# Kernel tuning notes

Measured on AMD Instinct MI355X. Metric: run time of the kernel, lower is better.

The kernel has to match this reference:

```python
import jax, jax.numpy as jnp
import numpy as np

N_NODES = 50000
N_EDGES = 800000
D_IN = 128
D_HID = 128
D_OUT = 128
EPS = 0.1  # GINConv eps


def setup_inputs() -> dict:
    key = jax.random.key(0)
    k = jax.random.split(key, 8)
    scale = 1.0 / np.sqrt(D_IN)
    return {
        "x": jax.random.normal(k[0], (N_NODES, D_IN), dtype=jnp.float32),
        "edge_index": jax.random.randint(k[1], (2, N_EDGES), 0, N_NODES, dtype=jnp.int64),
        "edge_weight": jax.random.uniform(k[2], (N_EDGES,), dtype=jnp.float32),
        "W1a": jax.random.normal(k[3], (D_IN, D_HID), dtype=jnp.float32) * scale,
        "W1b": jax.random.normal(k[4], (D_HID, D_HID), dtype=jnpp.float32) if False else jax.random.normal(k[4], (D_HID, D_HID), dtype=jnp.float32) * scale,
        "W2a": jax.random.normal(k[5], (D_HID, D_HID), dtype=jnp.float32) * scale,
        "W2b": jax.random.normal(k[6], (D_HID, D_OUT), dtype=jnp.float32) * scale,
    }


def _gin_conv(h, src, dst, ew, Wa, Wb, n_nodes):
    # edge-weighted neighbor sum: aggr[i] = sum_{(j->i)} w_ji * h[j]
    msg = ew[:, None] * h[src]                       # [E, d]
    aggr = jax.ops.segment_sum(msg, dst, num_segments=n_nodes)  # [N, d]
    z = (1.0 + EPS) * h + aggr                       # GIN update
    # 2-layer bias-free MLP: lin -> relu -> lin
    return jnp.maximum(z @ Wa, 0.0) @ Wb


def reference(x, edge_index, edge_weight, W1a, W1b, W2a, W2b):
    src, dst = edge_index[0], edge_index[1]
    n = x.shape[0]
    h = _gin_conv(x, src, dst, edge_weight, W1a, W1b, n)
    h = jnp.maximum(h, 0.0)  # relu between convs; dropout is identity in eval
    h = _gin_conv(h, src, dst, edge_weight, W2a, W2b, n)
    return h
```

## Files before the change

### kernel.cpp

```cpp
#include <hip/hip_runtime.h>
#include <hip/hip_fp16.h>

#define D 128
#define N_NODES 50000
#define EPSP1 1.1f

#define NPB 128
#define NBUCK 391
#define CAP 2560
#define P1E 4096
#define TS 136

typedef __attribute__((ext_vector_type(8))) short short8;
typedef __attribute__((ext_vector_type(4))) float f32x4;

__device__ __forceinline__ unsigned short f2bf(float f) {
    unsigned u = __float_as_uint(f);
    u += 0x7FFF + ((u >> 16) & 1);
    return (unsigned short)(u >> 16);
}
__device__ __forceinline__ float bf2f(unsigned short h) {
    return __uint_as_float(((unsigned)h) << 16);
}

__global__ __launch_bounds__(512, 4) void pass1_all(
    const int* __restrict__ src, const int* __restrict__ dst,
    const float* __restrict__ ew, int* __restrict__ gcnt,
    uint2* __restrict__ gstage, int ne, int nb1,
    const float* __restrict__ x, unsigned short* __restrict__ hb,
    int n4, int ncvt,
    const float* __restrict__ W1a, const float* __restrict__ W1b,
    const float* __restrict__ W2a, const float* __restrict__ W2b,
    unsigned short* __restrict__ wp)
{
    __shared__ int bcnt[NBUCK];
    __shared__ int goff[NBUCK];
    int tid = threadIdx.x;
    int bid = blockIdx.x;

    if (bid < nb1) {
        for (int i = tid; i < NBUCK; i += 512) bcnt[i] = 0;
        __syncthreads();
        int e0 = bid * P1E;
        int   rank[8];
        int   buck[8];
        uint2 pay[8];
#pragma unroll
        for (int j = 0; j < 8; ++j) {
            int e = e0 + j * 512 + tid;
            buck[j] = -1;
            if (e < ne) {
                int d_ = dst[e];
                int b  = d_ >> 7;
                int dl = d_ & 127;
                pay[j].x = (unsigned)(src[e] & 0xFFFF) | ((unsigned)dl << 16);
                pay[j].y = (unsigned)__half_as_ushort(__float2half_rn(ew[e]));
                rank[j]  = atomicAdd(&bcnt[b], 1);
                buck[j]  = b;
            }
        }
        __syncthreads();
        for (int i = tid; i < NBUCK; i += 512)
            if (bcnt[i] > 0) goff[i] = atomicAdd(&gcnt[i], bcnt[i]);
        __syncthreads();
#pragma unroll
        for (int j = 0; j < 8; ++j) {
            if (buck[j] >= 0) {
                int pos = goff[buck[j]] + rank[j];
                if (pos < CAP)
                    gstage[(size_t)buck[j] * CAP + pos] = pay[j];
            }
        }
    } else if (bid < nb1 + ncvt) {
        int base = (bid - nb1) * 4096;
#pragma unroll
        for (int it = 0; it < 8; ++it) {
            int i = base + it * 512 + tid;
            if (i < n4) {
                float4 v = ((const float4*)x)[i];
                ushort4 o;
                o.x = f2bf(v.x); o.y = f2bf(v.y); o.z = f2bf(v.z); o.w = f2bf(v.w);
                ((ushort4*)hb)[i] = o;
            }
        }
    } else {
        int e2 = (bid - nb1 - ncvt) * 512 + tid;
        if (e2 < 8192) {
            int mat = e2 >> 11;
            int e   = e2 & 2047;
            const float* W = (mat == 0) ? W1a : (mat == 1) ? W1b : (mat == 2) ? W2a : W2b;
            unsigned short* Wp = wp + (size_t)mat * 16384;
            int col = e & 127;
            int kq  = e >> 7;
            short8 v;
#pragma unroll
            for (int j = 0; j < 8; ++j)
                v[j] = (short)f2bf(W[(size_t)(kq * 8 + j) * 128 + col]);
            ((short8*)Wp)[e] = v;
        }
    }
}

__global__ __launch_bounds__(512) void csr_build(
    const uint2* __restrict__ gstage, const int* __restrict__ gcnt,
    unsigned* __restrict__ epay, int* __restrict__ off)
{
    __shared__ int hist[NPB];
    __shared__ int scn[NPB];
    __shared__ int exc[NPB];
    __shared__ int wtot[2];
    __shared__ int base_s;

    int b = blockIdx.x;
    int t = threadIdx.x;
    int cnt = min(gcnt[b], CAP);

    if (t < NPB) hist[t] = 0;
    __syncthreads();

    uint2 ent[CAP / 512];
    int   rnk[CAP / 512];
#pragma unroll
    for (int it = 0; it < CAP / 512; ++it) {
        int i = it * 512 + t;
        if (i < cnt) {
            ent[it] = gstage[(size_t)b * CAP + i];
            rnk[it] = atomicAdd(&hist[(ent[it].x >> 16) & 255], 1);
        }
    }
    __syncthreads();

    int w = t >> 6, l = t & 63;
    if (w < 2) {
        int v = hist[w * 64 + l];
#pragma unroll
        for (int dd = 1; dd < 64; dd <<= 1) {
            int u = __shfl_up(v, dd, 64);
            if (l >= dd) v += u;
        }
        scn[w * 64 + l] = v;
        if (l == 63) wtot[w] = v;
    } else if (w == 2) {
        int v = 0;
        for (int i = l; i < NBUCK; i += 64)
            if (i < b) v += min(gcnt[i], CAP);
#pragma unroll
        for (int dd = 32; dd > 0; dd >>= 1) v += __shfl_down(v, dd, 64);
        if (l == 0) base_s = v;
    }
    __syncthreads();

    if (t < NPB) {
        int pre = (t >= 64) ? wtot[0] : 0;
        int incl = scn[t] + pre;
        int excl = incl - hist[t];
        int node = (b << 7) + t;
        if (node <= N_NODES) off[node] = base_s + excl;
        exc[t] = excl;
    }
    __syncthreads();

    int base_s_r = base_s;
#pragma unroll
    for (int it = 0; it < CAP / 512; ++it) {
        int i = it * 512 + t;
        if (i < cnt) {
            int dl = (ent[it].x >> 16) & 255;
            epay[base_s_r + exc[dl] + rnk[it]] =
                (ent[it].x & 0xFFFF) | (ent[it].y << 16);
        }
    }
}

template<int RELU2, int OUT_F32>
__global__ __launch_bounds__(512, 8) void conv_fused(
    const unsigned short* __restrict__ h, const int* __restrict__ off,
    const unsigned* __restrict__ epay,
    const unsigned short* __restrict__ WpA,
    const unsigned short* __restrict__ WpB,
    void* __restrict__ outv, int n)
{
    __shared__ unsigned short t1[32 * TS];
    __shared__ unsigned short t2[32 * TS];
    __shared__ int offs[33];

    int tid  = threadIdx.x;
    int wave = tid >> 6;
    int lane = tid & 63;
    int qtr  = lane >> 4;
    int sub  = lane & 15;
    int nb   = blockIdx.x * 32;

    if (tid < 33) offs[tid] = off[min(nb + tid, n)];
    __syncthreads();

    int row  = wave * 4 + qtr;
    int node = nb + row;
    int beg = offs[row];
    int end = offs[row + 1];

    float acc[8];
#pragma unroll
    for (int c = 0; c < 8; ++c) acc[c] = 0.f;

    int i = beg;
    for (; i + 8 <= end; i += 8) {
        unsigned p0 = epay[i];
        unsigned p1 = epay[i + 1];
        unsigned p2 = epay[i + 2];
        unsigned p3 = epay[i + 3];
        unsigned p4 = epay[i + 4];
        unsigned p5 = epay[i + 5];
        unsigned p6 = epay[i + 6];
        unsigned p7 = epay[i + 7];
        short8 v0 = ((const short8*)(h + (size_t)(p0 & 0xFFFF) * D))[sub];
        short8 v1 = ((const short8*)(h + (size_t)(p1 & 0xFFFF) * D))[sub];
        short8 v2 = ((const short8*)(h + (size_t)(p2 & 0xFFFF) * D))[sub];
        short8 v3 = ((const short8*)(h + (size_t)(p3 & 0xFFFF) * D))[sub];
        short8 v4 = ((const short8*)(h + (size_t)(p4 & 0xFFFF) * D))[sub];
        short8 v5 = ((const short8*)(h + (size_t)(p5 & 0xFFFF) * D))[sub];
        short8 v6 = ((const short8*)(h + (size_t)(p6 & 0xFFFF) * D))[sub];
        short8 v7 = ((const short8*)(h + (size_t)(p7 & 0xFFFF) * D))[sub];
        float w0 = __half2float(__ushort_as_half((unsigned short)(p0 >> 16)));
        float w1 = __half2float(__ushort_as_half((unsigned short)(p1 >> 16)));
        float w2 = __half2float(__ushort_as_half((unsigned short)(p2 >> 16)));
        float w3 = __half2float(__ushort_as_half((unsigned short)(p3 >> 16)));
        float w4 = __half2float(__ushort_as_half((unsigned short)(p4 >> 16)));
        float w5 = __half2float(__ushort_as_half((unsigned short)(p5 >> 16)));
        float w6 = __half2float(__ushort_as_half((unsigned short)(p6 >> 16)));
        float w7 = __half2float(__ushort_as_half((unsigned short)(p7 >> 16)));
#pragma unroll
        for (int c = 0; c < 8; ++c)
            acc[c] += w0 * bf2f((unsigned short)v0[c]) + w1 * bf2f((unsigned short)v1[c])
                    + w2 * bf2f((unsigned short)v2[c]) + w3 * bf2f((unsigned short)v3[c])
                    + w4 * bf2f((unsigned short)v4[c]) + w5 * bf2f((unsigned short)v5[c])
                    + w6 * bf2f((unsigned short)v6[c]) + w7 * bf2f((unsigned short)v7[c]);
    }
    for (; i + 4 <= end; i += 4) {
        unsigned p0 = epay[i];
        unsigned p1 = epay[i + 1];
        unsigned p2 = epay[i + 2];
        unsigned p3 = epay[i + 3];
        short8 v0 = ((const short8*)(h + (size_t)(p0 & 0xFFFF) * D))[sub];
        short8 v1 = ((const short8*)(h + (size_t)(p1 & 0xFFFF) * D))[sub];
        short8 v2 = ((const short8*)(h + (size_t)(p2 & 0xFFFF) * D))[sub];
        short8 v3 = ((const short8*)(h + (size_t)(p3 & 0xFFFF) * D))[sub];
        float w0 = __half2float(__ushort_as_half((unsigned short)(p0 >> 16)));
        float w1 = __half2float(__ushort_as_half((unsigned short)(p1 >> 16)));
        float w2 = __half2float(__ushort_as_half((unsigned short)(p2 >> 16)));
        float w3 = __half2float(__ushort_as_half((unsigned short)(p3 >> 16)));
#pragma unroll
        for (int c = 0; c < 8; ++c)
            acc[c] += w0 * bf2f((unsigned short)v0[c]) + w1 * bf2f((unsigned short)v1[c])
                    + w2 * bf2f((unsigned short)v2[c]) + w3 * bf2f((unsigned short)v3[c]);
    }
    for (; i < end; ++i) {
        unsigned p0 = epay[i];
        short8 v0 = ((const short8*)(h + (size_t)(p0 & 0xFFFF) * D))[sub];
        float w0 = __half2float(__ushort_as_half((unsigned short)(p0 >> 16)));
#pragma unroll
        for (int c = 0; c < 8; ++c)
            acc[c] += w0 * bf2f((unsigned short)v0[c]);
    }

    {
        const short8 zero8 = {0, 0, 0, 0, 0, 0, 0, 0};
        short8 o;
        if (node < n) {
            short8 xv = ((const short8*)(h + (size_t)node * D))[sub];
#pragma unroll
            for (int c = 0; c < 8; ++c)
                o[c] = (short)f2bf(acc[c] + EPSP1 * bf2f((unsigned short)xv[c]));
        } else {
            o = zero8;
        }
        *(short8*)&t1[row * TS + sub * 8] = o;
    }
    __syncthreads();

    int cf = wave;
    f32x4 acc2[2];
    acc2[0] = (f32x4){0.f, 0.f, 0.f, 0.f};
    acc2[1] = (f32x4){0.f, 0.f, 0.f, 0.f};

#pragma unroll
    for (int kk = 0; kk < 4; ++kk) {
        short8 a0 = *(const short8*)&t1[(sub)      * TS + kk * 32 + qtr * 8];
        short8 a1 = *(const short8*)&t1[(16 + sub) * TS + kk * 32 + qtr * 8];
        short8 b  = *(const short8*)(WpA + ((size_t)(kk * 4 + qtr) * 128 + cf * 16 + sub) * 8);
        acc2[0] = __builtin_amdgcn_mfma_f32_16x16x32_bf16(a0, b, acc2[0], 0, 0, 0);
        acc2[1] = __builtin_amdgcn_mfma_f32_16x16x32_bf16(a1, b, acc2[1], 0, 0, 0);
    }

#pragma unroll
    for (int s = 0; s < 2; ++s)
#pragma unroll
        for (int reg = 0; reg < 4; ++reg) {
            int r = s * 16 + qtr * 4 + reg;
            t2[r * TS + cf * 16 + sub] = f2bf(fmaxf(acc2[s][reg], 0.f));
        }
    __syncthreads();

    acc2[0] = (f32x4){0.f, 0.f, 0.f, 0.f};
    acc2[1] = (f32x4){0.f, 0.f, 0.f, 0.f};

#pragma unroll
    for (int kk = 0; kk < 4; ++kk) {
        short8 a0 = *(const short8*)&t2[(sub)      * TS + kk * 32 + qtr * 8];
        short8 a1 = *(const short8*)&t2[(16 + sub) * TS + kk * 32 + qtr * 8];
        short8 b  = *(const short8*)(WpB + ((size_t)(kk * 4 + qtr) * 128 + cf * 16 + sub) * 8);
        acc2[0] = __builtin_amdgcn_mfma_f32_16x16x32_bf16(a0, b, acc2[0], 0, 0, 0);
        acc2[1] = __builtin_amdgcn_mfma_f32_16x16x32_bf16(a1, b, acc2[1], 0, 0, 0);
    }

#pragma unroll
    for (int s = 0; s < 2; ++s)
#pragma unroll
        for (int reg = 0; reg < 4; ++reg) {
            int r = nb + s * 16 + qtr * 4 + reg;
            if (r < n) {
                float v = acc2[s][reg];
                if (RELU2) v = fmaxf(v, 0.f);
                int col = cf * 16 + sub;
                if (OUT_F32)
                    ((float*)outv)[(size_t)r * D + col] = v;
                else
                    ((unsigned short*)outv)[(size_t)r * D + col] = f2bf(v);
            }
        }
}

extern "C" void kernel_launch(void* const* d_in, const int* in_sizes, int n_in,
                              void* d_out, int out_size, void* d_ws, size_t ws_size,
                              hipStream_t stream) {
    const float* x   = (const float*)d_in[0];
    const int*   ei  = (const int*)d_in[1];
    const float* ew  = (const float*)d_in[2];
    const float* W1a = (const float*)d_in[3];
    const float* W1b = (const float*)d_in[4];
    const float* W2a = (const float*)d_in[5];
    const float* W2b = (const float*)d_in[6];
    float* out = (float*)d_out;

    int n_edges = in_sizes[2];
    const int* src = ei;
    const int* dst = ei + n_edges;

    size_t node_elems = (size_t)N_NODES * D;
    unsigned short* hb = (unsigned short*)d_ws;
    unsigned short* zb = hb + node_elems;
    unsigned short* wp = zb + node_elems;
    unsigned* epay = (unsigned*)(wp + 4 * 16384);
    uint2*  gstage = (uint2*)(epay + n_edges);
    int*    gcnt   = (int*)(gstage + (size_t)NBUCK * CAP);
    int*    off    = gcnt + NBUCK;

    int nb1   = (n_edges + P1E - 1) / P1E;
    int n4    = (int)(node_elems / 4);
    int ncvt  = (n4 + 4095) / 4096;
    int npack = 16;
    int cgrid = (N_NODES + 31) / 32;

    hipMemsetAsync(gcnt, 0, NBUCK * sizeof(int), stream);

    pass1_all<<<nb1 + ncvt + npack, 512, 0, stream>>>(
        src, dst, ew, gcnt, gstage, n_edges, nb1,
        x, hb, n4, ncvt, W1a, W1b, W2a, W2b, wp);

    csr_build<<<NBUCK, 512, 0, stream>>>(gstage, gcnt, epay, off);

    unsigned short* wp0 = wp;
    unsigned short* wp1 = wp + 16384;
    unsigned short* wp2 = wp + 2 * 16384;
    unsigned short* wp3 = wp + 3 * 16384;

    conv_fused<1, 0><<<cgrid, 512, 0, stream>>>(hb, off, epay, wp0, wp1, zb, N_NODES);

    conv_fused<0, 1><<<cgrid, 512, 0, stream>>>(zb, off, epay, wp2, wp3, out, N_NODES);
}
```

Measured before the change: 192.1 us.

## Fuse CSR build into conv kernels via per-block LDS counting sort

Shrinks destination buckets to 32 nodes so each conv block owns one bucket, then sorts that bucket's staged edges by local node inside shared memory. This removes the separate csr_build kernel and its global epay/off writes and reads. In exchange the sort is redone in both conv layers, and pass1 uses more buckets with a smaller capacity, which risks dropping edges if a bucket overflows.

```diff
diff --git a/kernel.cpp b/kernel.cpp
--- a/kernel.cpp
+++ b/kernel.cpp
@@ -5,9 +5,9 @@
 #define N_NODES 50000
 #define EPSP1 1.1f
 
-#define NPB 128
-#define NBUCK 391
-#define CAP 2560
+#define NPB 32
+#define NBUCK 1563
+#define CAP 768
 #define P1E 4096
 #define TS 136
 
@@ -51,8 +51,8 @@
             buck[j] = -1;
             if (e < ne) {
                 int d_ = dst[e];
-                int b  = d_ >> 7;
-                int dl = d_ & 127;
+                int b  = d_ >> 5;
+                int dl = d_ & 31;
                 pay[j].x = (unsigned)(src[e] & 0xFFFF) | ((unsigned)dl << 16);
                 pay[j].y = (unsigned)__half_as_ushort(__float2half_rn(ew[e]));
                 rank[j]  = atomicAdd(&bcnt[b], 1);
@@ -101,103 +101,68 @@
     }
 }
 
-__global__ __launch_bounds__(512) void csr_build(
-    const uint2* __restrict__ gstage, const int* __restrict__ gcnt,
-    unsigned* __restrict__ epay, int* __restrict__ off)
-{
-    __shared__ int hist[NPB];
-    __shared__ int scn[NPB];
-    __shared__ int exc[NPB];
-    __shared__ int wtot[2];
-    __shared__ int base_s;
-
-    int b = blockIdx.x;
-    int t = threadIdx.x;
-    int cnt = min(gcnt[b], CAP);
-
-    if (t < NPB) hist[t] = 0;
-    __syncthreads();
-
-    uint2 ent[CAP / 512];
-    int   rnk[CAP / 512];
-#pragma unroll
-    for (int it = 0; it < CAP / 512; ++it) {
-        int i = it * 512 + t;
-        if (i < cnt) {
-            ent[it] = gstage[(size_t)b * CAP + i];
-            rnk[it] = atomicAdd(&hist[(ent[it].x >> 16) & 255], 1);
-        }
-    }
-    __syncthreads();
-
-    int w = t >> 6, l = t & 63;
-    if (w < 2) {
-        int v = hist[w * 64 + l];
-#pragma unroll
-        for (int dd = 1; dd < 64; dd <<= 1) {
-            int u = __shfl_up(v, dd, 64);
-            if (l >= dd) v += u;
-        }
-        scn[w * 64 + l] = v;
-        if (l == 63) wtot[w] = v;
-    } else if (w == 2) {
-        int v = 0;
-        for (int i = l; i < NBUCK; i += 64)
-            if (i < b) v += min(gcnt[i], CAP);
-#pragma unroll
-        for (int dd = 32; dd > 0; dd >>= 1) v += __shfl_down(v, dd, 64);
-        if (l == 0) base_s = v;
-    }
-    __syncthreads();
-
-    if (t < NPB) {
-        int pre = (t >= 64) ? wtot[0] : 0;
-        int incl = scn[t] + pre;
-        int excl = incl - hist[t];
-        int node = (b << 7) + t;
-        if (node <= N_NODES) off[node] = base_s + excl;
-        exc[t] = excl;
-    }
-    __syncthreads();
-
-    int base_s_r = base_s;
-#pragma unroll
-    for (int it = 0; it < CAP / 512; ++it) {
-        int i = it * 512 + t;
-        if (i < cnt) {
-            int dl = (ent[it].x >> 16) & 255;
-            epay[base_s_r + exc[dl] + rnk[it]] =
-                (ent[it].x & 0xFFFF) | (ent[it].y << 16);
-        }
-    }
-}
-
 template<int RELU2, int OUT_F32>
 __global__ __launch_bounds__(512, 8) void conv_fused(
-    const unsigned short* __restrict__ h, const int* __restrict__ off,
-    const unsigned* __restrict__ epay,
+    const unsigned short* __restrict__ h,
+    const uint2* __restrict__ gstage, const int* __restrict__ gcnt,
     const unsigned short* __restrict__ WpA,
     const unsigned short* __restrict__ WpB,
     void* __restrict__ outv, int n)
 {
     __shared__ unsigned short t1[32 * TS];
     __shared__ unsigned short t2[32 * TS];
-    __shared__ int offs[33];
+    __shared__ unsigned srt[CAP];
+    __shared__ int hist[NPB];
+    __shared__ int exc[NPB];
 
     int tid  = threadIdx.x;
     int wave = tid >> 6;
     int lane = tid & 63;
     int qtr  = lane >> 4;
     int sub  = lane & 15;
-    int nb   = blockIdx.x * 32;
-
-    if (tid < 33) offs[tid] = off[min(nb + tid, n)];
+    int b    = blockIdx.x;
+    int nb   = b * 32;
+
+    int cnt = min(gcnt[b], CAP);
+    if (tid < NPB) hist[tid] = 0;
+    __syncthreads();
+
+    uint2 ent[2];
+    int   rnk[2];
+    int   dl_[2];
+#pragma unroll
+    for (int it = 0; it < 2; ++it) {
+        int i = it * 512 + tid;
+        dl_[it] = -1;
+        if (i < cnt) {
+            ent[it] = gstage[(size_t)b * CAP + i];
+            dl_[it] = (ent[it].x >> 16) & 31;
+            rnk[it] = atomicAdd(&hist[dl_[it]], 1);
+        }
+    }
+    __syncthreads();
+
+    if (tid < NPB) {
+        int v = hist[tid];
+#pragma unroll
+        for (int dd = 1; dd < NPB; dd <<= 1) {
+            int u = __shfl_up(v, dd, 64);
+            if (tid >= dd) v += u;
+        }
+        exc[tid] = v - hist[tid];
+    }
+    __syncthreads();
+
+#pragma unroll
+    for (int it = 0; it < 2; ++it)
+        if (dl_[it] >= 0)
+            srt[exc[dl_[it]] + rnk[it]] = (ent[it].x & 0xFFFF) | (ent[it].y << 16);
     __syncthreads();
 
     int row  = wave * 4 + qtr;
     int node = nb + row;
-    int beg = offs[row];
-    int end = offs[row + 1];
+    int beg = exc[row];
+    int end = beg + hist[row];
 
     float acc[8];
 #pragma unroll
@@ -205,14 +170,14 @@
 
     int i = beg;
     for (; i + 8 <= end; i += 8) {
-        unsigned p0 = epay[i];
-        unsigned p1 = epay[i + 1];
-        unsigned p2 = epay[i + 2];
-        unsigned p3 = epay[i + 3];
-        unsigned p4 = epay[i + 4];
-        unsigned p5 = epay[i + 5];
-        unsigned p6 = epay[i + 6];
-        unsigned p7 = epay[i + 7];
+        unsigned p0 = srt[i];
+        unsigned p1 = srt[i + 1];
+        unsigned p2 = srt[i + 2];
+        unsigned p3 = srt[i + 3];
+        unsigned p4 = srt[i + 4];
+        unsigned p5 = srt[i + 5];
+        unsigned p6 = srt[i + 6];
+        unsigned p7 = srt[i + 7];
         short8 v0 = ((const short8*)(h + (size_t)(p0 & 0xFFFF) * D))[sub];
         short8 v1 = ((const short8*)(h + (size_t)(p1 & 0xFFFF) * D))[sub];
         short8 v2 = ((const short8*)(h + (size_t)(p2 & 0xFFFF) * D))[sub];
@@ -237,10 +202,10 @@
                     + w6 * bf2f((unsigned short)v6[c]) + w7 * bf2f((unsigned short)v7[c]);
     }
     for (; i + 4 <= end; i += 4) {
-        unsigned p0 = epay[i];
-        unsigned p1 = epay[i + 1];
-        unsigned p2 = epay[i + 2];
-        unsigned p3 = epay[i + 3];
+        unsigned p0 = srt[i];
+        unsigned p1 = srt[i + 1];
+        unsigned p2 = srt[i + 2];
+        unsigned p3 = srt[i + 3];
         short8 v0 = ((const short8*)(h + (size_t)(p0 & 0xFFFF) * D))[sub];
         short8 v1 = ((const short8*)(h + (size_t)(p1 & 0xFFFF) * D))[sub];
         short8 v2 = ((const short8*)(h + (size_t)(p2 & 0xFFFF) * D))[sub];
@@ -255,7 +220,7 @@
                     + w2 * bf2f((unsigned short)v2[c]) + w3 * bf2f((unsigned short)v3[c]);
     }
     for (; i < end; ++i) {
-        unsigned p0 = epay[i];
+        unsigned p0 = srt[i];
         short8 v0 = ((const short8*)(h + (size_t)(p0 & 0xFFFF) * D))[sub];
         float w0 = __half2float(__ushort_as_half((unsigned short)(p0 >> 16)));
 #pragma unroll
@@ -287,9 +252,9 @@
     for (int kk = 0; kk < 4; ++kk) {
         short8 a0 = *(const short8*)&t1[(sub)      * TS + kk * 32 + qtr * 8];
         short8 a1 = *(const short8*)&t1[(16 + sub) * TS + kk * 32 + qtr * 8];
-        short8 b  = *(const short8*)(WpA + ((size_t)(kk * 4 + qtr) * 128 + cf * 16 + sub) * 8);
-        acc2[0] = __builtin_amdgcn_mfma_f32_16x16x32_bf16(a0, b, acc2[0], 0, 0, 0);
-        acc2[1] = __builtin_amdgcn_mfma_f32_16x16x32_bf16(a1, b, acc2[1], 0, 0, 0);
+        short8 bb = *(const short8*)(WpA + ((size_t)(kk * 4 + qtr) * 128 + cf * 16 + sub) * 8);
+        acc2[0] = __builtin_amdgcn_mfma_f32_16x16x32_bf16(a0, bb, acc2[0], 0, 0, 0);
+        acc2[1] = __builtin_amdgcn_mfma_f32_16x16x32_bf16(a1, bb, acc2[1], 0, 0, 0);
     }
 
 #pragma unroll
@@ -308,9 +273,9 @@
     for (int kk = 0; kk < 4; ++kk) {
         short8 a0 = *(const short8*)&t2[(sub)      * TS + kk * 32 + qtr * 8];
         short8 a1 = *(const short8*)&t2[(16 + sub) * TS + kk * 32 + qtr * 8];
-        short8 b  = *(const short8*)(WpB + ((size_t)(kk * 4 + qtr) * 128 + cf * 16 + sub) * 8);
-        acc2[0] = __builtin_amdgcn_mfma_f32_16x16x32_bf16(a0, b, acc2[0], 0, 0, 0);
-        acc2[1] = __builtin_amdgcn_mfma_f32_16x16x32_bf16(a1, b, acc2[1], 0, 0, 0);
+        short8 bb = *(const short8*)(WpB + ((size_t)(kk * 4 + qtr) * 128 + cf * 16 + sub) * 8);
+        acc2[0] = __builtin_amdgcn_mfma_f32_16x16x32_bf16(a0, bb, acc2[0], 0, 0, 0);
+        acc2[1] = __builtin_amdgcn_mfma_f32_16x16x32_bf16(a1, bb, acc2[1], 0, 0, 0);
     }
 
 #pragma unroll
@@ -350,31 +315,27 @@
     unsigned short* hb = (unsigned short*)d_ws;
     unsigned short* zb = hb + node_elems;
     unsigned short* wp = zb + node_elems;
-    unsigned* epay = (unsigned*)(wp + 4 * 16384);
-    uint2*  gstage = (uint2*)(epay + n_edges);
+    uint2*  gstage = (uint2*)(wp + 4 * 16384);
     int*    gcnt   = (int*)(gstage + (size_t)NBUCK * CAP);
-    int*    off    = gcnt + NBUCK;
 
     int nb1   = (n_edges + P1E - 1) / P1E;
     int n4    = (int)(node_elems / 4);
     int ncvt  = (n4 + 4095) / 4096;
     int npack = 16;
-    int cgrid = (N_NODES + 31) / 32;
+    int cgrid = NBUCK;
 
     hipMemsetAsync(gcnt, 0, NBUCK * sizeof(int), stream);
 
     pass1_all<<<nb1 + ncvt + npack, 512, 0, stream>>>(
         src, dst, ew, gcnt, gstage, n_edges, nb1,
         x, hb, n4, ncvt, W1a, W1b, W2a, W2b, wp);
-
-    csr_build<<<NBUCK, 512, 0, stream>>>(gstage, gcnt, epay, off);
 
     unsigned short* wp0 = wp;
     unsigned short* wp1 = wp + 16384;
     unsigned short* wp2 = wp + 2 * 16384;
     unsigned short* wp3 = wp + 3 * 16384;
 
-    conv_fused<1, 0><<<cgrid, 512, 0, stream>>>(hb, off, epay, wp0, wp1, zb, N_NODES);
-
-    conv_fused<0, 1><<<cgrid, 512, 0, stream>>>(zb, off, epay, wp2, wp3, out, N_NODES);
-}
+    conv_fused<1, 0><<<cgrid, 512, 0, stream>>>(hb, gstage, gcnt, wp0, wp1, zb, N_NODES);
+
+    conv_fused<0, 1><<<cgrid, 512, 0, stream>>>(zb, gstage, gcnt, wp2, wp3, out, N_NODES);
+}
```

After: 179.3 us. -6.7%, faster.

## Drop counter memset via self-resetting device counters and stage CSR writes in LDS

Applied to the files above, without the earlier changes.

Replaces the workspace bucket-counter array and its per-call hipMemsetAsync with a device-global counter array. The last csr_build block to finish, detected with a done counter, zeroes it for the next call. csr_build now scatters entries into an LDS buffer with per-destination atomic cursors and then writes epay contiguously, replacing the scattered global stores. This removes one launch and gives coalesced writes, but relies on the reset protocol staying correct across calls and adds 10KB of LDS per block.

```diff
diff --git a/kernel.cpp b/kernel.cpp
--- a/kernel.cpp
+++ b/kernel.cpp
@@ -23,9 +23,12 @@
     return __uint_as_float(((unsigned)h) << 16);
 }
 
+__device__ int      gcnt_d[NBUCK];
+__device__ unsigned done_d;
+
 __global__ __launch_bounds__(512, 4) void pass1_all(
     const int* __restrict__ src, const int* __restrict__ dst,
-    const float* __restrict__ ew, int* __restrict__ gcnt,
+    const float* __restrict__ ew,
     uint2* __restrict__ gstage, int ne, int nb1,
     const float* __restrict__ x, unsigned short* __restrict__ hb,
     int n4, int ncvt,
@@ -61,7 +64,7 @@
         }
         __syncthreads();
         for (int i = tid; i < NBUCK; i += 512)
-            if (bcnt[i] > 0) goff[i] = atomicAdd(&gcnt[i], bcnt[i]);
+            if (bcnt[i] > 0) goff[i] = atomicAdd(&gcnt_d[i], bcnt[i]);
         __syncthreads();
 #pragma unroll
         for (int j = 0; j < 8; ++j) {
@@ -102,30 +105,31 @@
 }
 
 __global__ __launch_bounds__(512) void csr_build(
-    const uint2* __restrict__ gstage, const int* __restrict__ gcnt,
+    const uint2* __restrict__ gstage,
     unsigned* __restrict__ epay, int* __restrict__ off)
 {
     __shared__ int hist[NPB];
     __shared__ int scn[NPB];
-    __shared__ int exc[NPB];
+    __shared__ int loc[NPB];
     __shared__ int wtot[2];
     __shared__ int base_s;
+    __shared__ int lastf;
+    __shared__ unsigned csr[CAP];
 
     int b = blockIdx.x;
     int t = threadIdx.x;
-    int cnt = min(gcnt[b], CAP);
+    int cnt = min(gcnt_d[b], CAP);
 
     if (t < NPB) hist[t] = 0;
     __syncthreads();
 
     uint2 ent[CAP / 512];
-    int   rnk[CAP / 512];
 #pragma unroll
     for (int it = 0; it < CAP / 512; ++it) {
         int i = it * 512 + t;
         if (i < cnt) {
             ent[it] = gstage[(size_t)b * CAP + i];
-            rnk[it] = atomicAdd(&hist[(ent[it].x >> 16) & 255], 1);
+            atomicAdd(&hist[(ent[it].x >> 16) & 255], 1);
         }
     }
     __syncthreads();
@@ -143,7 +147,7 @@
     } else if (w == 2) {
         int v = 0;
         for (int i = l; i < NBUCK; i += 64)
-            if (i < b) v += min(gcnt[i], CAP);
+            if (i < b) v += min(gcnt_d[i], CAP);
 #pragma unroll
         for (int dd = 32; dd > 0; dd >>= 1) v += __shfl_down(v, dd, 64);
         if (l == 0) base_s = v;
@@ -156,20 +160,33 @@
         int excl = incl - hist[t];
         int node = (b << 7) + t;
         if (node <= N_NODES) off[node] = base_s + excl;
-        exc[t] = excl;
-    }
-    __syncthreads();
-
-    int base_s_r = base_s;
+        loc[t] = excl;
+    }
+    __syncthreads();
+
 #pragma unroll
     for (int it = 0; it < CAP / 512; ++it) {
         int i = it * 512 + t;
         if (i < cnt) {
             int dl = (ent[it].x >> 16) & 255;
-            epay[base_s_r + exc[dl] + rnk[it]] =
-                (ent[it].x & 0xFFFF) | (ent[it].y << 16);
-        }
-    }
+            int p = atomicAdd(&loc[dl], 1);
+            csr[p] = (ent[it].x & 0xFFFF) | (ent[it].y << 16);
+        }
+    }
+    __syncthreads();
+
+    for (int i = t; i < cnt; i += 512)
+        epay[base_s + i] = csr[i];
+
+    __syncthreads();
+    if (t == 0) {
+        __threadfence();
+        unsigned old = atomicAdd(&done_d, 1u);
+        lastf = ((old + 1u) % (unsigned)NBUCK == 0u) ? 1 : 0;
+    }
+    __syncthreads();
+    if (lastf)
+        for (int i = t; i < NBUCK; i += 512) gcnt_d[i] = 0;
 }
 
 template<int RELU2, int OUT_F32>
@@ -287,9 +304,9 @@
     for (int kk = 0; kk < 4; ++kk) {
         short8 a0 = *(const short8*)&t1[(sub)      * TS + kk * 32 + qtr * 8];
         short8 a1 = *(const short8*)&t1[(16 + sub) * TS + kk * 32 + qtr * 8];
-        short8 b  = *(const short8*)(WpA + ((size_t)(kk * 4 + qtr) * 128 + cf * 16 + sub) * 8);
-        acc2[0] = __builtin_amdgcn_mfma_f32_16x16x32_bf16(a0, b, acc2[0], 0, 0, 0);
-        acc2[1] = __builtin_amdgcn_mfma_f32_16x16x32_bf16(a1, b, acc2[1], 0, 0, 0);
+        short8 bb = *(const short8*)(WpA + ((size_t)(kk * 4 + qtr) * 128 + cf * 16 + sub) * 8);
+        acc2[0] = __builtin_amdgcn_mfma_f32_16x16x32_bf16(a0, bb, acc2[0], 0, 0, 0);
+        acc2[1] = __builtin_amdgcn_mfma_f32_16x16x32_bf16(a1, bb, acc2[1], 0, 0, 0);
     }
 
 #pragma unroll
@@ -308,9 +325,9 @@
     for (int kk = 0; kk < 4; ++kk) {
         short8 a0 = *(const short8*)&t2[(sub)      * TS + kk * 32 + qtr * 8];
         short8 a1 = *(const short8*)&t2[(16 + sub) * TS + kk * 32 + qtr * 8];
-        short8 b  = *(const short8*)(WpB + ((size_t)(kk * 4 + qtr) * 128 + cf * 16 + sub) * 8);
-        acc2[0] = __builtin_amdgcn_mfma_f32_16x16x32_bf16(a0, b, acc2[0], 0, 0, 0);
-        acc2[1] = __builtin_amdgcn_mfma_f32_16x16x32_bf16(a1, b, acc2[1], 0, 0, 0);
+        short8 bb = *(const short8*)(WpB + ((size_t)(kk * 4 + qtr) * 128 + cf * 16 + sub) * 8);
+        acc2[0] = __builtin_amdgcn_mfma_f32_16x16x32_bf16(a0, bb, acc2[0], 0, 0, 0);
+        acc2[1] = __builtin_amdgcn_mfma_f32_16x16x32_bf16(a1, bb, acc2[1], 0, 0, 0);
     }
 
 #pragma unroll
@@ -351,9 +368,8 @@
     unsigned short* zb = hb + node_elems;
     unsigned short* wp = zb + node_elems;
     unsigned* epay = (unsigned*)(wp + 4 * 16384);
-    uint2*  gstage = (uint2*)(epay + n_edges);
-    int*    gcnt   = (int*)(gstage + (size_t)NBUCK * CAP);
-    int*    off    = gcnt + NBUCK;
+    int*    off    = (int*)(epay + n_edges);
+    uint2*  gstage = (uint2*)(off + N_NODES + 1);
 
     int nb1   = (n_edges + P1E - 1) / P1E;
     int n4    = (int)(node_elems / 4);
@@ -361,13 +377,11 @@
     int npack = 16;
     int cgrid = (N_NODES + 31) / 32;
 
-    hipMemsetAsync(gcnt, 0, NBUCK * sizeof(int), stream);
-
     pass1_all<<<nb1 + ncvt + npack, 512, 0, stream>>>(
-        src, dst, ew, gcnt, gstage, n_edges, nb1,
+        src, dst, ew, gstage, n_edges, nb1,
         x, hb, n4, ncvt, W1a, W1b, W2a, W2b, wp);
 
-    csr_build<<<NBUCK, 512, 0, stream>>>(gstage, gcnt, epay, off);
+    csr_build<<<NBUCK, 512, 0, stream>>>(gstage, epay, off);
 
     unsigned short* wp0 = wp;
     unsigned short* wp1 = wp + 16384;
```

Measured after the change: 197.7 us. 2.9% more time.
